# Kernel optimization log

Measured on AMD Instinct MI355X. Metric: run time of the kernel, lower is better.

The kernel has to match this reference:

```python
import jax, jax.numpy as jnp
import numpy as np

B, S, E, H = 4, 2048, 2048, 1  # batch, seq, n_embd, n_head (source only runs with H=1)
LN_EPS = 1e-5


def _layernorm(x, g, b):
    m = jnp.mean(x, axis=-1, keepdims=True)
    v = jnp.mean(jnp.square(x - m), axis=-1, keepdims=True)
    return (x - m) * jax.lax.rsqrt(v + LN_EPS) * g + b


def setup_inputs() -> dict:
    key = jax.random.key(0)
    ks = jax.random.split(key, 8)
    sc = 0.02
    return {
        "x": jax.random.normal(ks[0], (B, S, E), jnp.float32),
        "mask": jnp.ones((B, S, 1, 1), jnp.int32),
        # attention params (torch Linear stored transposed: (in, out))
        "w_attn": jax.random.normal(ks[1], (E, H * E), jnp.float32) * sc,
        "b_attn": jnp.zeros((H * E,), jnp.float32),
        "w_kv": jax.random.normal(ks[2], (E, H * E), jnp.float32) * sc,
        "b_kv": jnp.zeros((H * E,), jnp.float32),
        "ln1_g": jnp.ones((E,), jnp.float32),
        "ln1_b": jnp.zeros((E,), jnp.float32),
        # MLP params
        "w_fc": jax.random.normal(ks[3], (E, 4 * E), jnp.float32) * sc,
        "b_fc": jnp.zeros((4 * E,), jnp.float32),
        "w_mproj": jax.random.normal(ks[4], (4 * E, E), jnp.float32) * sc,
        "b_mproj": jnp.zeros((E,), jnp.float32),
        "ln2_g": jnp.ones((E,), jnp.float32),
        "ln2_b": jnp.zeros((E,), jnp.float32),
    }


def reference(x, mask, w_attn, b_attn, w_kv, b_kv, ln1_g, ln1_b,
              w_fc, b_fc, w_mproj, b_mproj, ln2_g, ln2_b):
    # ---- Attention (faithful to source: einsum binds 'h' to the seq axis) ----
    h_attn = (x @ w_attn + b_attn).reshape(B, S, H, E)  # (b, s, h, d)
    h_proj = (x @ w_kv + b_kv).reshape(B, S, H, E)      # (b, s, h, d)
    # score[b, s, m, l] = sum_d h_attn[b, s, l, d] * h_proj[b, s, m, d]
    attn_score = jnp.einsum('bhld,bhmd->bhml', h_attn, h_proj)  # (B, S, H, H)
    attn_score = jnp.where(mask == 0, jnp.float32(-1e9), attn_score)
    attn_prob = jax.nn.softmax(attn_score, axis=-1)
    attn_vec = jnp.einsum('bhml,bhmd->bhld', attn_prob, h_proj)  # (B, S, H, E)
    attn_out = attn_vec.reshape(B, S, H * E)
    # (dropouts are identity in eval mode)
    # ---- Residual + LN + MLP + Residual + LN ----
    h = _layernorm(x + attn_out, ln1_g, ln1_b)
    h_mlp = jax.nn.gelu(h @ w_fc + b_fc, approximate=False)
    h_mlp = h_mlp @ w_mproj + b_mproj
    return _layernorm(h_mlp + x, ln2_g, ln2_b)
```

## Files before the change

kernel.cpp:

```cpp
#include <hip/hip_runtime.h>
#include <hip/hip_bf16.h>
#include <stdint.h>


typedef __attribute__((ext_vector_type(4))) float f32x4;
typedef __attribute__((ext_vector_type(8))) __bf16 bf16x8;
typedef __attribute__((ext_vector_type(8))) unsigned short ushort8;

__device__ __forceinline__ unsigned short f2bf(float f) {
  unsigned int u = __float_as_uint(f);
  return (unsigned short)((u + 0x7FFFu + ((u >> 16) & 1u)) >> 16);
}

__device__ __forceinline__ void gload_lds16(const void* g, void* l) {
  __builtin_amdgcn_global_load_lds(
      (const __attribute__((address_space(1))) unsigned int*)(uintptr_t)g,
      (__attribute__((address_space(3))) unsigned int*)(unsigned int)(uintptr_t)l,
      16, 0, 0);
}

__global__ __launch_bounds__(256) void cvt_bf16_kernel(
    const float* __restrict__ in, unsigned short* __restrict__ out, int n8) {
  int i = blockIdx.x * 256 + threadIdx.x;
  if (i >= n8) return;
  const size_t base = (size_t)i * 8;
  float4 a = *(const float4*)(in + base);
  float4 b = *(const float4*)(in + base + 4);
  ushort8 o;
  o[0] = f2bf(a.x); o[1] = f2bf(a.y); o[2] = f2bf(a.z); o[3] = f2bf(a.w);
  o[4] = f2bf(b.x); o[5] = f2bf(b.y); o[6] = f2bf(b.z); o[7] = f2bf(b.w);
  *(ushort8*)(out + base) = o;
}

__global__ __launch_bounds__(256) void transpose_cvt(
    const float* __restrict__ W, unsigned short* __restrict__ WT, int R, int C) {
  __shared__ unsigned short t[64][66];
  const int c0 = blockIdx.x * 64, r0 = blockIdx.y * 64;
  const int tid = threadIdx.x;
  const int lr = tid >> 4;
  const int lc = (tid & 15) * 4;
#pragma unroll
  for (int p = 0; p < 4; ++p) {
    const int r = lr + p * 16;
    float4 v = *(const float4*)(W + (size_t)(r0 + r) * C + c0 + lc);
    t[r][lc + 0] = f2bf(v.x);
    t[r][lc + 1] = f2bf(v.y);
    t[r][lc + 2] = f2bf(v.z);
    t[r][lc + 3] = f2bf(v.w);
  }
  __syncthreads();
#pragma unroll
  for (int p = 0; p < 4; ++p) {
    const int oc = lr + p * 16;
    ushort4 o;
    o.x = t[lc + 0][oc];
    o.y = t[lc + 1][oc];
    o.z = t[lc + 2][oc];
    o.w = t[lc + 3][oc];
    *(ushort4*)(WT + (size_t)(c0 + oc) * R + r0 + lc) = o;
  }
}

template <int EPI>
__global__ __launch_bounds__(512, 2) void gemm256(
    const unsigned short* __restrict__ A, const unsigned short* __restrict__ BT,
    const float* __restrict__ bias, const float* __restrict__ xres,
    void* __restrict__ out, int N, int K) {
  __shared__ unsigned short lds[2][2][256 * 64];

  const int tid = threadIdx.x;
  const int lane = tid & 63;
  const int w = tid >> 6;
  const int wm = w >> 2;
  const int wn = w & 3;

  const int nbn = N / 256;
  const int nwg = gridDim.x;
  const int bid = blockIdx.x;
  const int wg = (bid & 7) * (nwg >> 3) + (bid >> 3);
  const int bm = wg / nbn, bn = wg % nbn;

  const int nt = K / 64;

  const int srow = w * 8 + (lane >> 3);
  const int schunk = (lane & 7) ^ ((lane >> 3) & 7);
  const unsigned short* gA = A + (size_t)(bm * 256 + srow) * K + schunk * 8;
  const unsigned short* gB = BT + (size_t)(bn * 256 + srow) * K + schunk * 8;

  auto STAGE = [&](int buf, int op, int half, int tile) {
    const int tc = tile < nt ? tile : nt - 1;
    const unsigned short* g =
        (op ? gB : gA) + (size_t)(half * 128) * K + (size_t)tc * 64;
    unsigned short* l = &lds[buf][op][(half * 128 + w * 8) * 64];
    gload_lds16(g, l);
    gload_lds16(g + (size_t)64 * K, l + 64 * 64);
  };

  const int rA = wm * 128 + (lane & 15);
  const int rB = wn * 64 + (lane & 15);
  const int kq = lane >> 4;
  const int x7 = lane & 7;

  auto LDA = [&](int buf, int mh, int mf, int ks) -> bf16x8 {
    const char* p = (const char*)&lds[buf][0][0] +
                    (rA + mh * 64 + mf * 16) * 128 +
                    (((ks * 4 + kq) ^ x7) << 4);
    return *(const bf16x8*)p;
  };
  auto LDB = [&](int buf, int nh, int nf, int ks) -> bf16x8 {
    const char* p = (const char*)&lds[buf][1][0] +
                    (rB + nh * 32 + nf * 16) * 128 +
                    (((ks * 4 + kq) ^ x7) << 4);
    return *(const bf16x8*)p;
  };

  f32x4 acc[8][4] = {};
  bf16x8 aLo[4][2], aHi[4][2], bfr[2][2];

  STAGE(0, 0, 0, 0); STAGE(0, 0, 1, 0); STAGE(0, 1, 0, 0); STAGE(0, 1, 1, 0);
  STAGE(1, 0, 0, 1); STAGE(1, 0, 1, 1); STAGE(1, 1, 0, 1);
  asm volatile("s_waitcnt vmcnt(6)" ::: "memory");
  __builtin_amdgcn_s_barrier();

  for (int t = 0; t < nt; ++t) {
    const int cb = t & 1, ob = cb ^ 1;
#pragma unroll
    for (int mf = 0; mf < 4; ++mf)
#pragma unroll
      for (int ks = 0; ks < 2; ++ks) aLo[mf][ks] = LDA(cb, 0, mf, ks);
#pragma unroll
    for (int nf = 0; nf < 2; ++nf)
#pragma unroll
      for (int ks = 0; ks < 2; ++ks) bfr[nf][ks] = LDB(cb, 0, nf, ks);
    STAGE(ob, 1, 1, t + 1);
    __builtin_amdgcn_s_barrier();
    asm volatile("s_waitcnt lgkmcnt(0)" ::: "memory");
    __builtin_amdgcn_sched_barrier(0);
    __builtin_amdgcn_s_setprio(1);
#pragma unroll
    for (int mf = 0; mf < 4; ++mf)
#pragma unroll
      for (int nf = 0; nf < 2; ++nf)
#pragma unroll
        for (int ks = 0; ks < 2; ++ks)
          acc[mf][nf] = __builtin_amdgcn_mfma_f32_16x16x32_bf16(
              aLo[mf][ks], bfr[nf][ks], acc[mf][nf], 0, 0, 0);
    __builtin_amdgcn_s_setprio(0);
    __builtin_amdgcn_s_barrier();
#pragma unroll
    for (int mf = 0; mf < 4; ++mf)
#pragma unroll
      for (int ks = 0; ks < 2; ++ks) aHi[mf][ks] = LDA(cb, 1, mf, ks);
    __builtin_amdgcn_s_barrier();
    asm volatile("s_waitcnt lgkmcnt(0)" ::: "memory");
    __builtin_amdgcn_sched_barrier(0);
    __builtin_amdgcn_s_setprio(1);
#pragma unroll
    for (int mf = 0; mf < 4; ++mf)
#pragma unroll
      for (int nf = 0; nf < 2; ++nf)
#pragma unroll
        for (int ks = 0; ks < 2; ++ks)
          acc[4 + mf][nf] = __builtin_amdgcn_mfma_f32_16x16x32_bf16(
              aHi[mf][ks], bfr[nf][ks], acc[4 + mf][nf], 0, 0, 0);
    __builtin_amdgcn_s_setprio(0);
    __builtin_amdgcn_s_barrier();
#pragma unroll
    for (int nf = 0; nf < 2; ++nf)
#pragma unroll
      for (int ks = 0; ks < 2; ++ks) bfr[nf][ks] = LDB(cb, 1, nf, ks);
    STAGE(cb, 0, 0, t + 2);
    __builtin_amdgcn_s_barrier();
    asm volatile("s_waitcnt lgkmcnt(0)" ::: "memory");
    __builtin_amdgcn_sched_barrier(0);
    __builtin_amdgcn_s_setprio(1);
#pragma unroll
    for (int mf = 0; mf < 4; ++mf)
#pragma unroll
      for (int nf = 0; nf < 2; ++nf)
#pragma unroll
        for (int ks = 0; ks < 2; ++ks)
          acc[4 + mf][2 + nf] = __builtin_amdgcn_mfma_f32_16x16x32_bf16(
              aHi[mf][ks], bfr[nf][ks], acc[4 + mf][2 + nf], 0, 0, 0);
    __builtin_amdgcn_s_setprio(0);
    __builtin_amdgcn_s_barrier();
    STAGE(cb, 0, 1, t + 2);
    STAGE(cb, 1, 0, t + 2);
    __builtin_amdgcn_s_barrier();
    __builtin_amdgcn_sched_barrier(0);
    __builtin_amdgcn_s_setprio(1);
#pragma unroll
    for (int mf = 0; mf < 4; ++mf)
#pragma unroll
      for (int nf = 0; nf < 2; ++nf)
#pragma unroll
        for (int ks = 0; ks < 2; ++ks)
          acc[mf][2 + nf] = __builtin_amdgcn_mfma_f32_16x16x32_bf16(
              aLo[mf][ks], bfr[nf][ks], acc[mf][2 + nf], 0, 0, 0);
    __builtin_amdgcn_s_setprio(0);
    asm volatile("s_waitcnt vmcnt(6)" ::: "memory");
    __builtin_amdgcn_s_barrier();
  }
  asm volatile("s_waitcnt vmcnt(0)" ::: "memory");

  const int col0 = bn * 256 + wn * 64 + (lane & 15);
  const int row0 = bm * 256 + wm * 128 + ((lane >> 4) << 2);
  float bv[4];
#pragma unroll
  for (int n = 0; n < 4; ++n) bv[n] = bias[col0 + n * 16];
#pragma unroll
  for (int mf = 0; mf < 8; ++mf) {
#pragma unroll
    for (int j = 0; j < 4; ++j) {
      const size_t row = (size_t)(row0 + mf * 16 + j);
#pragma unroll
      for (int n = 0; n < 4; ++n) {
        const size_t idx = row * N + col0 + n * 16;
        float v = acc[mf][n][j] + bv[n];
        if (EPI == 0) {
          ((float*)out)[idx] = v + xres[idx];
        } else {
          float ge = 0.5f * v * (1.0f + erff(v * 0.7071067811865475f));
          ((unsigned short*)out)[idx] = f2bf(ge);
        }
      }
    }
  }
}

template <int OUT_BF16>
__global__ __launch_bounds__(256) void ln_row(const float* __restrict__ tin,
                                              const float* __restrict__ gw,
                                              const float* __restrict__ bw,
                                              void* __restrict__ outp) {
  const int row = blockIdx.x;
  const int tid = threadIdx.x;
  const size_t base = (size_t)row * 2048 + tid * 8;
  alignas(16) float v[8];
  *(float4*)(v) = *(const float4*)(tin + base);
  *(float4*)(v + 4) = *(const float4*)(tin + base + 4);
  float s = 0.f, q = 0.f;
#pragma unroll
  for (int i = 0; i < 8; ++i) { s += v[i]; q += v[i] * v[i]; }
#pragma unroll
  for (int m = 32; m >= 1; m >>= 1) {
    s += __shfl_xor(s, m);
    q += __shfl_xor(q, m);
  }
  __shared__ float red[8];
  if ((tid & 63) == 0) {
    red[tid >> 6] = s;
    red[4 + (tid >> 6)] = q;
  }
  __syncthreads();
  s = red[0] + red[1] + red[2] + red[3];
  q = red[4] + red[5] + red[6] + red[7];
  const float mean = s * (1.0f / 2048.0f);
  float var = q * (1.0f / 2048.0f) - mean * mean;
  var = fmaxf(var, 0.0f);
  const float rstd = rsqrtf(var + 1e-5f);
  alignas(16) float gv[8], bv[8];
  *(float4*)(gv) = *(const float4*)(gw + (size_t)tid * 8);
  *(float4*)(gv + 4) = *(const float4*)(gw + (size_t)tid * 8 + 4);
  *(float4*)(bv) = *(const float4*)(bw + (size_t)tid * 8);
  *(float4*)(bv + 4) = *(const float4*)(bw + (size_t)tid * 8 + 4);
  if (OUT_BF16) {
    ushort8 o;
#pragma unroll
    for (int i = 0; i < 8; ++i)
      o[i] = f2bf((v[i] - mean) * rstd * gv[i] + bv[i]);
    *(ushort8*)((unsigned short*)outp + base) = o;
  } else {
    alignas(16) float r[8];
#pragma unroll
    for (int i = 0; i < 8; ++i) r[i] = (v[i] - mean) * rstd * gv[i] + bv[i];
    *(float4*)((float*)outp + base) = *(float4*)(r);
    *(float4*)((float*)outp + base + 4) = *(float4*)(r + 4);
  }
}

extern "C" void kernel_launch(void* const* d_in, const int* in_sizes, int n_in,
                              void* d_out, int out_size, void* d_ws,
                              size_t ws_size, hipStream_t stream) {
  constexpr int M = 8192;
  constexpr int E = 2048;
  constexpr int F = 8192;
  const size_t MiB = 1ull << 20;

  const float* x = (const float*)d_in[0];
  const float* w_kv = (const float*)d_in[4];
  const float* b_kv = (const float*)d_in[5];
  const float* ln1_g = (const float*)d_in[6];
  const float* ln1_b = (const float*)d_in[7];
  const float* w_fc = (const float*)d_in[8];
  const float* b_fc = (const float*)d_in[9];
  const float* w_mproj = (const float*)d_in[10];
  const float* b_mproj = (const float*)d_in[11];
  const float* ln2_g = (const float*)d_in[12];
  const float* ln2_b = (const float*)d_in[13];
  float* out = (float*)d_out;
  char* ws = (char*)d_ws;

  float* tbuf = out;

  int nch;
  unsigned short *xb, *wkvT, *wfcT, *wmpT, *hb, *gch;
  if (ws_size >= 224 * MiB) {
    nch = 1;
    gch = (unsigned short*)(ws + 0);
    xb = (unsigned short*)(ws + 0);
    wkvT = (unsigned short*)(ws + 32 * MiB);
    wfcT = (unsigned short*)(ws + 128 * MiB);
    wmpT = (unsigned short*)(ws + 160 * MiB);
    hb = (unsigned short*)(ws + 192 * MiB);
  } else if (ws_size >= 160 * MiB) {
    nch = 2;
    gch = (unsigned short*)(ws + 0);
    xb = (unsigned short*)(ws + 0);
    wkvT = (unsigned short*)(ws + 32 * MiB);
    hb = (unsigned short*)(ws + 64 * MiB);
    wfcT = (unsigned short*)(ws + 96 * MiB);
    wmpT = (unsigned short*)(ws + 128 * MiB);
  } else {
    nch = 4;
    gch = (unsigned short*)(ws + 0);
    xb = (unsigned short*)(ws + 0);
    wkvT = (unsigned short*)(ws + 32 * MiB);
    hb = (unsigned short*)(ws + 32 * MiB);
    wfcT = (unsigned short*)(ws + 64 * MiB);
    wmpT = (unsigned short*)(ws + 96 * MiB);
  }

  cvt_bf16_kernel<<<(M * E / 8 + 255) / 256, 256, 0, stream>>>(x, xb, M * E / 8);
  transpose_cvt<<<dim3(E / 64, E / 64), 256, 0, stream>>>(w_kv, wkvT, E, E);
  transpose_cvt<<<dim3(F / 64, E / 64), 256, 0, stream>>>(w_fc, wfcT, E, F);
  transpose_cvt<<<dim3(E / 64, F / 64), 256, 0, stream>>>(w_mproj, wmpT, F, E);

  gemm256<0><<<(M / 256) * (E / 256), 512, 0, stream>>>(xb, wkvT, b_kv, x,
                                                        tbuf, E, E);
  ln_row<1><<<M, 256, 0, stream>>>(tbuf, ln1_g, ln1_b, hb);
  const int Mc = M / nch;
  for (int c = 0; c < nch; ++c) {
    const size_t roff = (size_t)c * Mc;
    gemm256<1><<<(Mc / 256) * (F / 256), 512, 0, stream>>>(
        hb + roff * E, wfcT, b_fc, nullptr, gch, F, E);
    gemm256<0><<<(Mc / 256) * (E / 256), 512, 0, stream>>>(
        gch, wmpT, b_mproj, x + roff * E, tbuf + roff * E, E, F);
  }
  ln_row<0><<<M, 256, 0, stream>>>(tbuf, ln2_g, ln2_b, out);
}
```

Baseline: 706.3 us.

## Restructure GEMM main loop to prefetch LDS fragments across MFMA clusters

Rewrites the bf16 GEMM main loop so that the LDS fragment reads for the next cluster are issued before the current MFMA cluster runs. Partial lgkmcnt waits replace the full drains, and the A-low and B-low fragments for the next tile are prefetched at the end of each iteration. The global->LDS staging is reordered so that all four stages of tile t+2 are issued in the current iteration, with a vmcnt-based wait, and the separate ob-stage issue is removed. The goal is to hide LDS latency behind MFMAs and cut barrier stalls, at the cost of more live registers and a riskier hand-tuned wait-count ordering.

```diff
diff --git a/kernel.cpp b/kernel.cpp
--- a/kernel.cpp
+++ b/kernel.cpp
@@ -18,6 +18,11 @@
       (__attribute__((address_space(3))) unsigned int*)(unsigned int)(uintptr_t)l,
       16, 0, 0);
 }
+
+#define WAITLGK(n) asm volatile("s_waitcnt lgkmcnt(" #n ")" ::: "memory")
+#define WAITVM(n) asm volatile("s_waitcnt vmcnt(" #n ")" ::: "memory")
+#define SBAR() __builtin_amdgcn_s_barrier()
+#define SCHED0() __builtin_amdgcn_sched_barrier(0)
 
 __global__ __launch_bounds__(256) void cvt_bf16_kernel(
     const float* __restrict__ in, unsigned short* __restrict__ out, int n8) {
@@ -100,108 +105,91 @@
   const int rB = wn * 64 + (lane & 15);
   const int kq = lane >> 4;
   const int x7 = lane & 7;
-
-  auto LDA = [&](int buf, int mh, int mf, int ks) -> bf16x8 {
-    const char* p = (const char*)&lds[buf][0][0] +
-                    (rA + mh * 64 + mf * 16) * 128 +
-                    (((ks * 4 + kq) ^ x7) << 4);
-    return *(const bf16x8*)p;
-  };
-  auto LDB = [&](int buf, int nh, int nf, int ks) -> bf16x8 {
-    const char* p = (const char*)&lds[buf][1][0] +
-                    (rB + nh * 32 + nf * 16) * 128 +
-                    (((ks * 4 + kq) ^ x7) << 4);
-    return *(const bf16x8*)p;
-  };
+  const int c0 = ((kq ^ x7) << 4);
+  const int c1 = (((4 + kq) ^ x7) << 4);
 
   f32x4 acc[8][4] = {};
-  bf16x8 aLo[4][2], aHi[4][2], bfr[2][2];
+  bf16x8 aS0[4][2], aS1[4][2], b0v[2][2], b1v[2][2];
+
+#define READ_ALO(buf)                                              \
+  {                                                                \
+    const char* p = (const char*)&lds[buf][0][0] + rA * 128;       \
+    _Pragma("unroll") for (int mf = 0; mf < 4; ++mf) {             \
+      aS0[mf][0] = *(const bf16x8*)(p + mf * 2048 + c0);           \
+      aS0[mf][1] = *(const bf16x8*)(p + mf * 2048 + c1);           \
+    }                                                              \
+  }
+#define READ_AHI(buf)                                              \
+  {                                                                \
+    const char* p = (const char*)&lds[buf][0][0] + rA * 128 + 8192;\
+    _Pragma("unroll") for (int mf = 0; mf < 4; ++mf) {             \
+      aS1[mf][0] = *(const bf16x8*)(p + mf * 2048 + c0);           \
+      aS1[mf][1] = *(const bf16x8*)(p + mf * 2048 + c1);           \
+    }                                                              \
+  }
+#define READ_B0(buf)                                               \
+  {                                                                \
+    const char* p = (const char*)&lds[buf][1][0] + rB * 128;       \
+    _Pragma("unroll") for (int nf = 0; nf < 2; ++nf) {             \
+      b0v[nf][0] = *(const bf16x8*)(p + nf * 2048 + c0);           \
+      b0v[nf][1] = *(const bf16x8*)(p + nf * 2048 + c1);           \
+    }                                                              \
+  }
+#define READ_B1(buf)                                               \
+  {                                                                \
+    const char* p = (const char*)&lds[buf][1][0] + rB * 128 + 4096;\
+    _Pragma("unroll") for (int nf = 0; nf < 2; ++nf) {             \
+      b1v[nf][0] = *(const bf16x8*)(p + nf * 2048 + c0);           \
+      b1v[nf][1] = *(const bf16x8*)(p + nf * 2048 + c1);           \
+    }                                                              \
+  }
+#define CLUSTER(ASET, BSET, MO, NO)                                         \
+  __builtin_amdgcn_s_setprio(1);                                            \
+  _Pragma("unroll") for (int mf = 0; mf < 4; ++mf)                          \
+      _Pragma("unroll") for (int nf = 0; nf < 2; ++nf)                      \
+          _Pragma("unroll") for (int ks = 0; ks < 2; ++ks)                  \
+              acc[MO + mf][NO + nf] =                                       \
+                  __builtin_amdgcn_mfma_f32_16x16x32_bf16(                  \
+                      ASET[mf][ks], BSET[nf][ks], acc[MO + mf][NO + nf],    \
+                      0, 0, 0);                                             \
+  __builtin_amdgcn_s_setprio(0);
 
   STAGE(0, 0, 0, 0); STAGE(0, 0, 1, 0); STAGE(0, 1, 0, 0); STAGE(0, 1, 1, 0);
-  STAGE(1, 0, 0, 1); STAGE(1, 0, 1, 1); STAGE(1, 1, 0, 1);
-  asm volatile("s_waitcnt vmcnt(6)" ::: "memory");
-  __builtin_amdgcn_s_barrier();
+  STAGE(1, 0, 0, 1); STAGE(1, 0, 1, 1); STAGE(1, 1, 0, 1); STAGE(1, 1, 1, 1);
+  WAITVM(8);
+  SBAR();
+  READ_ALO(0);
+  READ_B0(0);
 
   for (int t = 0; t < nt; ++t) {
     const int cb = t & 1, ob = cb ^ 1;
-#pragma unroll
-    for (int mf = 0; mf < 4; ++mf)
-#pragma unroll
-      for (int ks = 0; ks < 2; ++ks) aLo[mf][ks] = LDA(cb, 0, mf, ks);
-#pragma unroll
-    for (int nf = 0; nf < 2; ++nf)
-#pragma unroll
-      for (int ks = 0; ks < 2; ++ks) bfr[nf][ks] = LDB(cb, 0, nf, ks);
-    STAGE(ob, 1, 1, t + 1);
-    __builtin_amdgcn_s_barrier();
-    asm volatile("s_waitcnt lgkmcnt(0)" ::: "memory");
-    __builtin_amdgcn_sched_barrier(0);
-    __builtin_amdgcn_s_setprio(1);
-#pragma unroll
-    for (int mf = 0; mf < 4; ++mf)
-#pragma unroll
-      for (int nf = 0; nf < 2; ++nf)
-#pragma unroll
-        for (int ks = 0; ks < 2; ++ks)
-          acc[mf][nf] = __builtin_amdgcn_mfma_f32_16x16x32_bf16(
-              aLo[mf][ks], bfr[nf][ks], acc[mf][nf], 0, 0, 0);
-    __builtin_amdgcn_s_setprio(0);
-    __builtin_amdgcn_s_barrier();
-#pragma unroll
-    for (int mf = 0; mf < 4; ++mf)
-#pragma unroll
-      for (int ks = 0; ks < 2; ++ks) aHi[mf][ks] = LDA(cb, 1, mf, ks);
-    __builtin_amdgcn_s_barrier();
-    asm volatile("s_waitcnt lgkmcnt(0)" ::: "memory");
-    __builtin_amdgcn_sched_barrier(0);
-    __builtin_amdgcn_s_setprio(1);
-#pragma unroll
-    for (int mf = 0; mf < 4; ++mf)
-#pragma unroll
-      for (int nf = 0; nf < 2; ++nf)
-#pragma unroll
-        for (int ks = 0; ks < 2; ++ks)
-          acc[4 + mf][nf] = __builtin_amdgcn_mfma_f32_16x16x32_bf16(
-              aHi[mf][ks], bfr[nf][ks], acc[4 + mf][nf], 0, 0, 0);
-    __builtin_amdgcn_s_setprio(0);
-    __builtin_amdgcn_s_barrier();
-#pragma unroll
-    for (int nf = 0; nf < 2; ++nf)
-#pragma unroll
-      for (int ks = 0; ks < 2; ++ks) bfr[nf][ks] = LDB(cb, 1, nf, ks);
+    READ_B1(cb);
+    WAITLGK(4);
+    SCHED0();
+    CLUSTER(aS0, b0v, 0, 0);
+    SBAR();
+    READ_AHI(cb);
+    WAITLGK(8);
+    SCHED0();
+    CLUSTER(aS0, b1v, 0, 2);
+    SBAR();
     STAGE(cb, 0, 0, t + 2);
-    __builtin_amdgcn_s_barrier();
-    asm volatile("s_waitcnt lgkmcnt(0)" ::: "memory");
-    __builtin_amdgcn_sched_barrier(0);
-    __builtin_amdgcn_s_setprio(1);
-#pragma unroll
-    for (int mf = 0; mf < 4; ++mf)
-#pragma unroll
-      for (int nf = 0; nf < 2; ++nf)
-#pragma unroll
-        for (int ks = 0; ks < 2; ++ks)
-          acc[4 + mf][2 + nf] = __builtin_amdgcn_mfma_f32_16x16x32_bf16(
-              aHi[mf][ks], bfr[nf][ks], acc[4 + mf][2 + nf], 0, 0, 0);
-    __builtin_amdgcn_s_setprio(0);
-    __builtin_amdgcn_s_barrier();
+    WAITLGK(0);
+    SCHED0();
+    CLUSTER(aS1, b0v, 4, 0);
+    WAITVM(2);
+    SBAR();
+    READ_ALO(ob);
+    READ_B0(ob);
     STAGE(cb, 0, 1, t + 2);
     STAGE(cb, 1, 0, t + 2);
-    __builtin_amdgcn_s_barrier();
-    __builtin_amdgcn_sched_barrier(0);
-    __builtin_amdgcn_s_setprio(1);
-#pragma unroll
-    for (int mf = 0; mf < 4; ++mf)
-#pragma unroll
-      for (int nf = 0; nf < 2; ++nf)
-#pragma unroll
-        for (int ks = 0; ks < 2; ++ks)
-          acc[mf][2 + nf] = __builtin_amdgcn_mfma_f32_16x16x32_bf16(
-              aLo[mf][ks], bfr[nf][ks], acc[mf][2 + nf], 0, 0, 0);
-    __builtin_amdgcn_s_setprio(0);
-    asm volatile("s_waitcnt vmcnt(6)" ::: "memory");
-    __builtin_amdgcn_s_barrier();
-  }
-  asm volatile("s_waitcnt vmcnt(0)" ::: "memory");
+    STAGE(cb, 1, 1, t + 2);
+    WAITLGK(12);
+    SCHED0();
+    CLUSTER(aS1, b1v, 4, 2);
+    SBAR();
+  }
+  WAITVM(0);
 
   const int col0 = bn * 256 + wn * 64 + (lane & 15);
   const int row0 = bm * 256 + wm * 128 + ((lane >> 4) << 2);
@@ -226,6 +214,11 @@
       }
     }
   }
+#undef READ_ALO
+#undef READ_AHI
+#undef READ_B0
+#undef READ_B1
+#undef CLUSTER
 }
 
 template <int OUT_BF16>
```

Measured after the change: 689.7 us. 1.02x faster.
